# Optimization experiments

Hardware: AMD Instinct MI355X
Metric: run time of the kernel (lower is better)

Reference implementation:

```python
import jax, jax.numpy as jnp
import numpy as np

B, T, M, P = 512, 128, 512, 512


def setup_inputs() -> dict:
    key = jax.random.key(0)
    ks = jax.random.split(key, 20)
    g = lambda k, shape: (jax.random.normal(k, shape, dtype=jnp.float32) * 0.02)
    return {
        "encoded_inputs": jax.random.normal(ks[0], (B, T, M), dtype=jnp.float32),
        "y": jax.random.normal(ks[1], (B, T, 1), dtype=jnp.float32),
        # W_d: Linear(2P, M)
        "W_d_w": g(ks[2], (M, 2 * P)), "W_d_b": g(ks[3], (M,)),
        # U_d: Linear(M, M, bias=False)
        "U_d_w": g(ks[4], (M, M)),
        # v_d: Linear(M, 1, bias=False)
        "v_d_w": g(ks[5], (1, M)),
        # w_tilda: Linear(M+1, 1)
        "w_tilda_w": g(ks[6], (1, M + 1)), "w_tilda_b": g(ks[7], (1,)),
        # W_y: Linear(P+M, P)
        "W_y_w": g(ks[8], (P, P + M)), "W_y_b": g(ks[9], (P,)),
        # v_y: Linear(P, 1)
        "v_y_w": g(ks[10], (1, P)), "v_y_b": g(ks[11], (1,)),
        # LSTMCell(input_size=1, hidden_size=P); gate order i, f, g, o
        "W_ih": g(ks[12], (4 * P, 1)), "W_hh": g(ks[13], (4 * P, P)),
        "b_ih": g(ks[14], (4 * P,)), "b_hh": g(ks[15], (4 * P,)),
    }


def _forward(encoded_inputs, y, W_d_w, W_d_b, U_d_w, v_d_w, w_tilda_w, w_tilda_b,
             W_y_w, W_y_b, v_y_w, v_y_b, W_ih, W_hh, b_ih, b_hh):
    Bn = encoded_inputs.shape[0]
    # U_d(encoded_inputs) is identical at every timestep in the original loop; hoist it.
    Uy = jnp.einsum('btm,nm->btn', encoded_inputs, U_d_w)  # [B,T,M]

    def step(carry, y_t):
        d, s, _ = carry  # d: hidden [B,P], s: cell [B,P]
        x1 = jnp.concatenate([d, s], axis=1) @ W_d_w.T + W_d_b       # [B,M]
        z1 = jnp.tanh(x1[:, None, :] + Uy)                           # [B,T,M]
        l = jnp.einsum('btm,m->bt', z1, v_d_w[0])                    # [B,T]
        beta = jax.nn.softmax(l, axis=1)
        c_t = jnp.einsum('bt,btm->bm', beta, encoded_inputs)          # [B,M]
        y_tilda = jnp.concatenate([c_t, y_t], axis=1) @ w_tilda_w.T + w_tilda_b  # [B,1]
        gates = y_tilda @ W_ih.T + b_ih + d @ W_hh.T + b_hh          # [B,4P]
        i_g, f_g, g_g, o_g = jnp.split(gates, 4, axis=1)
        i_g = jax.nn.sigmoid(i_g); f_g = jax.nn.sigmoid(f_g)
        g_g = jnp.tanh(g_g); o_g = jax.nn.sigmoid(o_g)
        s_new = f_g * s + i_g * g_g
        d_new = o_g * jnp.tanh(s_new)
        return (d_new, s_new, c_t), None

    init = (jnp.zeros((Bn, P), encoded_inputs.dtype),
            jnp.zeros((Bn, P), encoded_inputs.dtype),
            jnp.zeros((Bn, M), encoded_inputs.dtype))
    (d_T, s_T, c_T), _ = jax.lax.scan(step, init, jnp.swapaxes(y, 0, 1))  # scan over T
    h = jnp.concatenate([d_T, c_T], axis=1) @ W_y_w.T + W_y_b            # [B,P]
    return h @ v_y_w.T + v_y_b                                           # [B,1]


def reference(encoded_inputs, y, W_d_w, W_d_b, U_d_w, v_d_w, w_tilda_w, w_tilda_b,
              W_y_w, W_y_b, v_y_w, v_y_b, W_ih, W_hh, b_ih, b_hh):
    return _forward(encoded_inputs, y, W_d_w, W_d_b, U_d_w, v_d_w, w_tilda_w,
                    w_tilda_b, W_y_w, W_y_b, v_y_w, v_y_b, W_ih, W_hh, b_ih, b_hh)
```

## Files before the change

kernel.cpp:

```cpp
#include <hip/hip_runtime.h>
#include <hip/hip_bf16.h>

#define Bsz 512
#define Tsz 128
#define Msz 512
#define Psz 512

typedef __attribute__((ext_vector_type(8))) unsigned short ushort8v;
typedef __attribute__((ext_vector_type(8))) short short8v;
typedef __attribute__((ext_vector_type(4))) float floatx4;

__device__ __forceinline__ float h2f(unsigned short u) {
    union { unsigned short u; _Float16 h; } c; c.u = u; return (float)c.h;
}
__device__ __forceinline__ unsigned short f2h(float f) {
    union { unsigned short u; _Float16 h; } c; c.h = (_Float16)f; return c.u;
}
__device__ __forceinline__ unsigned short f2bf(float f) {
    union { float f; unsigned int i; } c; c.f = f;
    unsigned int u = c.i;
    unsigned int r = u + 0x7fffu + ((u >> 16) & 1u);
    return (unsigned short)(r >> 16);
}
__device__ __forceinline__ float fast_tanh(float x) {
    x = fminf(fmaxf(x, -15.f), 15.f);
    float e = __expf(2.f * x);
    return 1.f - 2.f / (e + 1.f);
}
__device__ __forceinline__ float fast_sig(float x) {
    x = fminf(fmaxf(x, -30.f), 30.f);
    return 1.f / (1.f + __expf(-x));
}

__global__ __launch_bounds__(256) void k_uy(const float* __restrict__ A,
                                            const float* __restrict__ U,
                                            unsigned short* __restrict__ C) {
    __shared__ float As[32][68];
    __shared__ float Us[32][68];
    const int tid = threadIdx.x;
    const int tx = tid & 15, ty = tid >> 4;
    const size_t r0 = (size_t)blockIdx.y * 64;
    const int n0 = blockIdx.x * 64;
    float acc[4][4] = {};
    for (int k0 = 0; k0 < 512; k0 += 32) {
#pragma unroll
        for (int i = 0; i < 2; ++i) {
            int f = tid + i * 256;
            int r = f >> 3;
            int kc = (f & 7) * 4;
            float4 v = *reinterpret_cast<const float4*>(&A[(r0 + r) * 512 + k0 + kc]);
            As[kc + 0][r] = v.x; As[kc + 1][r] = v.y; As[kc + 2][r] = v.z; As[kc + 3][r] = v.w;
            float4 w = *reinterpret_cast<const float4*>(&U[(size_t)(n0 + r) * 512 + k0 + kc]);
            Us[kc + 0][r] = w.x; Us[kc + 1][r] = w.y; Us[kc + 2][r] = w.z; Us[kc + 3][r] = w.w;
        }
        __syncthreads();
#pragma unroll
        for (int k = 0; k < 32; ++k) {
            float4 a = *reinterpret_cast<const float4*>(&As[k][ty * 4]);
            float4 b = *reinterpret_cast<const float4*>(&Us[k][tx * 4]);
            float av[4] = {a.x, a.y, a.z, a.w};
            float bv[4] = {b.x, b.y, b.z, b.w};
#pragma unroll
            for (int i = 0; i < 4; ++i)
#pragma unroll
                for (int j = 0; j < 4; ++j)
                    acc[i][j] = fmaf(av[i], bv[j], acc[i][j]);
        }
        __syncthreads();
    }
#pragma unroll
    for (int i = 0; i < 4; ++i) {
        size_t row = r0 + ty * 4 + i;
        ushort4 o;
        o.x = f2h(acc[i][0]); o.y = f2h(acc[i][1]);
        o.z = f2h(acc[i][2]); o.w = f2h(acc[i][3]);
        *reinterpret_cast<ushort4*>(&C[row * 512 + n0 + tx * 4]) = o;
    }
}

__global__ __launch_bounds__(256) void k_e2h(const float* __restrict__ e,
                                             unsigned short* __restrict__ o) {
    size_t i = ((size_t)blockIdx.x * 256 + threadIdx.x) * 8;
    float4 a = *reinterpret_cast<const float4*>(e + i);
    float4 b = *reinterpret_cast<const float4*>(e + i + 4);
    ushort8v r;
    r[0] = f2h(a.x); r[1] = f2h(a.y); r[2] = f2h(a.z); r[3] = f2h(a.w);
    r[4] = f2h(b.x); r[5] = f2h(b.y); r[6] = f2h(b.z); r[7] = f2h(b.w);
    *reinterpret_cast<ushort8v*>(o + i) = r;
}

__global__ __launch_bounds__(256) void k_w2b(const float* __restrict__ Whh,
                                             const float* __restrict__ Wdw,
                                             unsigned short* __restrict__ W16) {
    size_t o = ((size_t)blockIdx.x * 256 + threadIdx.x) * 8;
    int row = (int)(o >> 9), k = (int)(o & 511);
    const float* src;
    if (row < 2048)      src = &Whh[(size_t)row * 512 + k];
    else if (row < 2560) src = &Wdw[(size_t)(row - 2048) * 1024 + k];
    else                 src = &Wdw[(size_t)(row - 2560) * 1024 + 512 + k];
    float4 a = *reinterpret_cast<const float4*>(src);
    float4 b = *reinterpret_cast<const float4*>(src + 4);
    ushort8v r;
    r[0] = f2bf(a.x); r[1] = f2bf(a.y); r[2] = f2bf(a.z); r[3] = f2bf(a.w);
    r[4] = f2bf(b.x); r[5] = f2bf(b.y); r[6] = f2bf(b.z); r[7] = f2bf(b.w);
    *reinterpret_cast<ushort8v*>(W16 + o) = r;
}

__global__ void k_zero(float* a, float* b, unsigned short* ah, unsigned short* bh, int n) {
    int i = blockIdx.x * blockDim.x + threadIdx.x;
    if (i < n) { a[i] = 0.f; b[i] = 0.f; ah[i] = 0; bh[i] = 0; }
}

__global__ __launch_bounds__(256) void k_mm(const unsigned short* __restrict__ dbh,
                                            const unsigned short* __restrict__ sbh,
                                            const unsigned short* __restrict__ W16,
                                            const float* __restrict__ Wdb,
                                            float* __restrict__ gacc,
                                            float* __restrict__ x1g) {
    __shared__ unsigned short As[64][48];
    __shared__ unsigned short Ws[64][48];
    const int tid = threadIdx.x;
    const int lane = tid & 63, w = tid >> 6;
    const int rbw = (w >> 1) * 32, cbw = (w & 1) * 32;
    const int b0 = blockIdx.y * 64;
    const int n0 = blockIdx.x * 64;
    const bool isx1 = (n0 >= 2048);
    const int l15 = lane & 15, kq = (lane >> 4) * 8;
    floatx4 acc00 = {}, acc01 = {}, acc10 = {}, acc11 = {};

    const int npass = isx1 ? 2 : 1;
    for (int pass = 0; pass < npass; ++pass) {
        const unsigned short* Ab = (pass == 0) ? dbh : sbh;
        const unsigned short* Wb = W16 + (size_t)(pass == 0 ? n0 : n0 + 512) * 512;
        for (int k0 = 0; k0 < 512; k0 += 32) {
            {
                const int r = tid >> 2, kc = (tid & 3) * 8;
                *reinterpret_cast<ushort8v*>(&As[r][kc]) =
                    *reinterpret_cast<const ushort8v*>(&Ab[(size_t)(b0 + r) * 512 + k0 + kc]);
                *reinterpret_cast<ushort8v*>(&Ws[r][kc]) =
                    *reinterpret_cast<const ushort8v*>(&Wb[(size_t)r * 512 + k0 + kc]);
            }
            __syncthreads();
            short8v a0 = *reinterpret_cast<const short8v*>(&As[rbw + l15][kq]);
            short8v a1 = *reinterpret_cast<const short8v*>(&As[rbw + 16 + l15][kq]);
            short8v q0 = *reinterpret_cast<const short8v*>(&Ws[cbw + l15][kq]);
            short8v q1 = *reinterpret_cast<const short8v*>(&Ws[cbw + 16 + l15][kq]);
            acc00 = __builtin_amdgcn_mfma_f32_16x16x32_bf16(a0, q0, acc00, 0, 0, 0);
            acc01 = __builtin_amdgcn_mfma_f32_16x16x32_bf16(a0, q1, acc01, 0, 0, 0);
            acc10 = __builtin_amdgcn_mfma_f32_16x16x32_bf16(a1, q0, acc10, 0, 0, 0);
            acc11 = __builtin_amdgcn_mfma_f32_16x16x32_bf16(a1, q1, acc11, 0, 0, 0);
            __syncthreads();
        }
    }
    const int rB = rbw + (lane >> 4) * 4;
#pragma unroll
    for (int fr = 0; fr < 2; ++fr)
#pragma unroll
        for (int fc = 0; fc < 2; ++fc) {
            const floatx4 av = fr ? (fc ? acc11 : acc10) : (fc ? acc01 : acc00);
            const int col = cbw + fc * 16 + l15;
#pragma unroll
            for (int i = 0; i < 4; ++i) {
                const int row = b0 + rB + fr * 16 + i;
                if (!isx1) {
                    gacc[(size_t)row * 2048 + n0 + col] = av[i];
                } else {
                    const int m = (n0 - 2048) + col;
                    x1g[(size_t)row * 512 + m] = av[i] + Wdb[m];
                }
            }
        }
}

__global__ __launch_bounds__(512) void k_attn2(const unsigned short* __restrict__ Uyh,
                                               const unsigned short* __restrict__ ench,
                                               const float* __restrict__ encf,
                                               const float* __restrict__ x1g,
                                               const float* __restrict__ vd,
                                               const float* __restrict__ wt,
                                               const float* __restrict__ wtb,
                                               const float* __restrict__ yin,
                                               const float* __restrict__ gacc,
                                               const float* __restrict__ Wih,
                                               const float* __restrict__ bih,
                                               const float* __restrict__ bhh,
                                               const float* __restrict__ scur,
                                               float* __restrict__ snxt,
                                               float* __restrict__ dnxt,
                                               unsigned short* __restrict__ snh,
                                               unsigned short* __restrict__ dnh,
                                               float* __restrict__ cout,
                                               int tstep, int useh) {
    __shared__ float x1_s[512];
    __shared__ float l_s[128];
    __shared__ float pacc[8][512];
    __shared__ float sred[8];
    __shared__ float y_bc;
    const int tid = threadIdx.x, b = blockIdx.x;
    const int w = tid >> 6, lane = tid & 63;
    x1_s[tid] = x1g[(size_t)b * 512 + tid];
    __syncthreads();
    {
        const int mb = lane * 8;
        float4 xa = *reinterpret_cast<const float4*>(&x1_s[mb]);
        float4 xb = *reinterpret_cast<const float4*>(&x1_s[mb + 4]);
        float4 va = *reinterpret_cast<const float4*>(&vd[mb]);
        float4 vb = *reinterpret_cast<const float4*>(&vd[mb + 4]);
        const unsigned short* ubase = Uyh + (size_t)b * 128 * 512 + mb;
#pragma unroll 2
        for (int tt = 0; tt < 16; ++tt) {
            const int t = w * 16 + tt;
            ushort8v u = *reinterpret_cast<const ushort8v*>(ubase + (size_t)t * 512);
            float s;
            s  = fast_tanh(h2f(u[0]) + xa.x) * va.x;
            s += fast_tanh(h2f(u[1]) + xa.y) * va.y;
            s += fast_tanh(h2f(u[2]) + xa.z) * va.z;
            s += fast_tanh(h2f(u[3]) + xa.w) * va.w;
            s += fast_tanh(h2f(u[4]) + xb.x) * vb.x;
            s += fast_tanh(h2f(u[5]) + xb.y) * vb.y;
            s += fast_tanh(h2f(u[6]) + xb.z) * vb.z;
            s += fast_tanh(h2f(u[7]) + xb.w) * vb.w;
#pragma unroll
            for (int off = 32; off; off >>= 1) s += __shfl_xor(s, off);
            if (lane == 0) l_s[t] = s;
        }
    }
    __syncthreads();
    if (tid < 64) {
        float v0 = l_s[tid], v1 = l_s[tid + 64];
        float mx = fmaxf(v0, v1);
#pragma unroll
        for (int off = 32; off; off >>= 1) mx = fmaxf(mx, __shfl_xor(mx, off));
        float e0 = __expf(v0 - mx), e1 = __expf(v1 - mx);
        float sm = e0 + e1;
#pragma unroll
        for (int off = 32; off; off >>= 1) sm += __shfl_xor(sm, off);
        float inv = 1.f / sm;
        l_s[tid] = e0 * inv; l_s[tid + 64] = e1 * inv;
    }
    __syncthreads();
    float a0 = 0.f, a1 = 0.f, a2 = 0.f, a3 = 0.f, a4 = 0.f, a5 = 0.f, a6 = 0.f, a7 = 0.f;
    if (useh) {
        const unsigned short* eb = ench + (size_t)b * (Tsz * Msz) + lane * 8;
#pragma unroll
        for (int tt = 0; tt < 16; ++tt) {
            const int t = tt * 8 + w;
            ushort8v uu = *reinterpret_cast<const ushort8v*>(eb + (size_t)t * 512);
            const float bt = l_s[t];
            a0 = fmaf(bt, h2f(uu[0]), a0); a1 = fmaf(bt, h2f(uu[1]), a1);
            a2 = fmaf(bt, h2f(uu[2]), a2); a3 = fmaf(bt, h2f(uu[3]), a3);
            a4 = fmaf(bt, h2f(uu[4]), a4); a5 = fmaf(bt, h2f(uu[5]), a5);
            a6 = fmaf(bt, h2f(uu[6]), a6); a7 = fmaf(bt, h2f(uu[7]), a7);
        }
    } else {
        const float* eb = encf + (size_t)b * (Tsz * Msz) + lane * 8;
#pragma unroll
        for (int tt = 0; tt < 16; ++tt) {
            const int t = tt * 8 + w;
            float4 e0 = *reinterpret_cast<const float4*>(eb + (size_t)t * 512);
            float4 e1 = *reinterpret_cast<const float4*>(eb + (size_t)t * 512 + 4);
            const float bt = l_s[t];
            a0 = fmaf(bt, e0.x, a0); a1 = fmaf(bt, e0.y, a1);
            a2 = fmaf(bt, e0.z, a2); a3 = fmaf(bt, e0.w, a3);
            a4 = fmaf(bt, e1.x, a4); a5 = fmaf(bt, e1.y, a5);
            a6 = fmaf(bt, e1.z, a6); a7 = fmaf(bt, e1.w, a7);
        }
    }
    float* pr = &pacc[w][lane * 8];
    *reinterpret_cast<float4*>(pr)     = make_float4(a0, a1, a2, a3);
    *reinterpret_cast<float4*>(pr + 4) = make_float4(a4, a5, a6, a7);
    __syncthreads();
    float c = pacc[0][tid];
#pragma unroll
    for (int ww = 1; ww < 8; ++ww) c += pacc[ww][tid];
    cout[(size_t)b * 512 + tid] = c;
    float part = c * wt[tid];
#pragma unroll
    for (int off = 32; off; off >>= 1) part += __shfl_xor(part, off);
    if (lane == 0) sred[w] = part;
    __syncthreads();
    if (tid == 0) {
        float tot = sred[0] + sred[1] + sred[2] + sred[3] +
                    sred[4] + sred[5] + sred[6] + sred[7];
        y_bc = tot + yin[(size_t)b * 128 + tstep] * wt[512] + wtb[0];
    }
    __syncthreads();
    {
        const float yt = y_bc;
        const int p = tid;
        const int e = b * 512 + p;
        const float* ga = gacc + (size_t)b * 2048;
        float gi = ga[p]        + yt * Wih[p]        + bih[p]        + bhh[p];
        float gf = ga[512 + p]  + yt * Wih[512 + p]  + bih[512 + p]  + bhh[512 + p];
        float gg = ga[1024 + p] + yt * Wih[1024 + p] + bih[1024 + p] + bhh[1024 + p];
        float go = ga[1536 + p] + yt * Wih[1536 + p] + bih[1536 + p] + bhh[1536 + p];
        float sv = fast_sig(gf) * scur[e] + fast_sig(gi) * fast_tanh(gg);
        float dv = fast_sig(go) * fast_tanh(sv);
        snxt[e] = sv; dnxt[e] = dv;
        snh[e] = f2bf(sv); dnh[e] = f2bf(dv);
    }
}

__global__ __launch_bounds__(256) void k_final(const float* __restrict__ dfin,
                                               const float* __restrict__ cfin,
                                               const float* __restrict__ Wy,
                                               const float* __restrict__ Wyb,
                                               const float* __restrict__ vy,
                                               const float* __restrict__ vyb,
                                               float* __restrict__ out) {
    __shared__ float hc[1024];
    __shared__ float sred[8];
    const int tid = threadIdx.x, b = blockIdx.x;
    hc[tid] = dfin[(size_t)b * 512 + tid];
    hc[256 + tid] = dfin[(size_t)b * 512 + 256 + tid];
    hc[512 + tid] = cfin[(size_t)b * 512 + tid];
    hc[768 + tid] = cfin[(size_t)b * 512 + 256 + tid];
    __syncthreads();
    float part = 0.f;
#pragma unroll
    for (int pi = 0; pi < 2; ++pi) {
        int p = tid + pi * 256;
        float acc = Wyb[p];
        const float* wr = Wy + (size_t)p * 1024;
#pragma unroll 4
        for (int k = 0; k < 1024; k += 4) {
            float4 w = *reinterpret_cast<const float4*>(&wr[k]);
            acc = fmaf(hc[k], w.x, acc);
            acc = fmaf(hc[k + 1], w.y, acc);
            acc = fmaf(hc[k + 2], w.z, acc);
            acc = fmaf(hc[k + 3], w.w, acc);
        }
        part += acc * vy[p];
    }
#pragma unroll
    for (int off = 32; off; off >>= 1) part += __shfl_xor(part, off);
    const int lane = tid & 63, wid = tid >> 6;
    if (lane == 0) sred[wid] = part;
    __syncthreads();
    if (tid == 0) out[b] = sred[0] + sred[1] + sred[2] + sred[3] + vyb[0];
}

extern "C" void kernel_launch(void* const* d_in, const int* in_sizes, int n_in,
                              void* d_out, int out_size, void* d_ws, size_t ws_size,
                              hipStream_t stream) {
    const float* enc = (const float*)d_in[0];
    const float* yin = (const float*)d_in[1];
    const float* Wdw = (const float*)d_in[2];
    const float* Wdb = (const float*)d_in[3];
    const float* Udw = (const float*)d_in[4];
    const float* vdw = (const float*)d_in[5];
    const float* wtw = (const float*)d_in[6];
    const float* wtb = (const float*)d_in[7];
    const float* Wyw = (const float*)d_in[8];
    const float* Wyb = (const float*)d_in[9];
    const float* vyw = (const float*)d_in[10];
    const float* vyb = (const float*)d_in[11];
    const float* Wih = (const float*)d_in[12];
    const float* Whh = (const float*)d_in[13];
    const float* bih = (const float*)d_in[14];
    const float* bhh = (const float*)d_in[15];
    float* out = (float*)d_out;
    const int N = Bsz * Psz;

    char* p = (char*)d_ws;
    unsigned short* Uyh = (unsigned short*)p;  p += (size_t)Bsz * Tsz * Msz * 2;
    unsigned short* W16 = (unsigned short*)p;  p += (size_t)3072 * 512 * 2;
    unsigned short* dbh = (unsigned short*)p;  p += (size_t)2 * N * 2;
    unsigned short* sbh = (unsigned short*)p;  p += (size_t)2 * N * 2;
    float* dbuf = (float*)p;  p += (size_t)2 * N * 4;
    float* sbuf = (float*)p;  p += (size_t)2 * N * 4;
    float* x1g  = (float*)p;  p += (size_t)N * 4;
    float* cb   = (float*)p;  p += (size_t)N * 4;
    float* gacc = (float*)p;  p += (size_t)Bsz * 2048 * 4;
    unsigned short* ench = (unsigned short*)p;
    const size_t need = (size_t)((char*)(ench + (size_t)Bsz * Tsz * Msz) - (char*)d_ws);
    const int useh = (ws_size >= need) ? 1 : 0;

    k_uy<<<dim3(Msz / 64, (Bsz * Tsz) / 64), 256, 0, stream>>>(enc, Udw, Uyh);
    if (useh)
        k_e2h<<<(Bsz * Tsz * Msz) / (256 * 8), 256, 0, stream>>>(enc, ench);
    k_w2b<<<(3072 * 512) / (256 * 8), 256, 0, stream>>>(Whh, Wdw, W16);
    k_zero<<<(N + 255) / 256, 256, 0, stream>>>(dbuf, sbuf, dbh, sbh, N);

    for (int t = 0; t < Tsz; ++t) {
        const int c = t & 1, n = c ^ 1;
        k_mm<<<dim3(40, 8), 256, 0, stream>>>(dbh + (size_t)c * N, sbh + (size_t)c * N,
                                              W16, Wdb, gacc, x1g);
        k_attn2<<<Bsz, 512, 0, stream>>>(Uyh, ench, enc, x1g, vdw, wtw, wtb, yin,
                                         gacc, Wih, bih, bhh,
                                         sbuf + (size_t)c * N,
                                         sbuf + (size_t)n * N, dbuf + (size_t)n * N,
                                         sbh + (size_t)n * N, dbh + (size_t)n * N,
                                         cb, t, useh);
    }
    k_final<<<Bsz, 256, 0, stream>>>(dbuf, cb, Wyw, Wyb, vyw, vyb, out);
}
```

Baseline: 7.292 ms.

## Precompute encoder·w_tilda projection and only build context vector at last step

Since y_tilda = beta·(enc·w_tilda[:M]) + ..., the per-step context vector reduction over the full [T,M] encoder tile is replaced by a dot product of beta with a precomputed [B,T] projection computed once in a new kernel. The full weighted sum over encoder states is now only performed at the final timestep, where c_T is needed for the output head. This removes reading the fp16 encoder copy every step, drops the fp16 conversion kernel, and changes the summation order of y_tilda slightly.

```diff
diff --git a/kernel.cpp b/kernel.cpp
--- a/kernel.cpp
+++ b/kernel.cpp
@@ -78,15 +78,22 @@
     }
 }
 
-__global__ __launch_bounds__(256) void k_e2h(const float* __restrict__ e,
-                                             unsigned short* __restrict__ o) {
-    size_t i = ((size_t)blockIdx.x * 256 + threadIdx.x) * 8;
-    float4 a = *reinterpret_cast<const float4*>(e + i);
-    float4 b = *reinterpret_cast<const float4*>(e + i + 4);
-    ushort8v r;
-    r[0] = f2h(a.x); r[1] = f2h(a.y); r[2] = f2h(a.z); r[3] = f2h(a.w);
-    r[4] = f2h(b.x); r[5] = f2h(b.y); r[6] = f2h(b.z); r[7] = f2h(b.w);
-    *reinterpret_cast<ushort8v*>(o + i) = r;
+__global__ __launch_bounds__(256) void k_ewt(const float* __restrict__ enc,
+                                             const float* __restrict__ wt,
+                                             float* __restrict__ ewt) {
+    const int lane = threadIdx.x & 63;
+    const int pair = blockIdx.x * 4 + (threadIdx.x >> 6);
+    const float* e = enc + (size_t)pair * 512 + lane * 8;
+    float4 a = *reinterpret_cast<const float4*>(e);
+    float4 b = *reinterpret_cast<const float4*>(e + 4);
+    const float* wp = wt + lane * 8;
+    float4 w0 = *reinterpret_cast<const float4*>(wp);
+    float4 w1 = *reinterpret_cast<const float4*>(wp + 4);
+    float s = a.x * w0.x + a.y * w0.y + a.z * w0.z + a.w * w0.w +
+              b.x * w1.x + b.y * w1.y + b.z * w1.z + b.w * w1.w;
+#pragma unroll
+    for (int off = 32; off; off >>= 1) s += __shfl_xor(s, off);
+    if (lane == 0) ewt[pair] = s;
 }
 
 __global__ __launch_bounds__(256) void k_w2b(const float* __restrict__ Whh,
@@ -172,9 +179,9 @@
         }
 }
 
-__global__ __launch_bounds__(512) void k_attn2(const unsigned short* __restrict__ Uyh,
-                                               const unsigned short* __restrict__ ench,
+__global__ __launch_bounds__(512) void k_attn3(const unsigned short* __restrict__ Uyh,
                                                const float* __restrict__ encf,
+                                               const float* __restrict__ ewt,
                                                const float* __restrict__ x1g,
                                                const float* __restrict__ vd,
                                                const float* __restrict__ wt,
@@ -190,11 +197,10 @@
                                                unsigned short* __restrict__ snh,
                                                unsigned short* __restrict__ dnh,
                                                float* __restrict__ cout,
-                                               int tstep, int useh) {
+                                               int tstep) {
     __shared__ float x1_s[512];
     __shared__ float l_s[128];
     __shared__ float pacc[8][512];
-    __shared__ float sred[8];
     __shared__ float y_bc;
     const int tid = threadIdx.x, b = blockIdx.x;
     const int w = tid >> 6, lane = tid & 63;
@@ -239,21 +245,17 @@
         l_s[tid] = e0 * inv; l_s[tid + 64] = e1 * inv;
     }
     __syncthreads();
-    float a0 = 0.f, a1 = 0.f, a2 = 0.f, a3 = 0.f, a4 = 0.f, a5 = 0.f, a6 = 0.f, a7 = 0.f;
-    if (useh) {
-        const unsigned short* eb = ench + (size_t)b * (Tsz * Msz) + lane * 8;
-#pragma unroll
-        for (int tt = 0; tt < 16; ++tt) {
-            const int t = tt * 8 + w;
-            ushort8v uu = *reinterpret_cast<const ushort8v*>(eb + (size_t)t * 512);
-            const float bt = l_s[t];
-            a0 = fmaf(bt, h2f(uu[0]), a0); a1 = fmaf(bt, h2f(uu[1]), a1);
-            a2 = fmaf(bt, h2f(uu[2]), a2); a3 = fmaf(bt, h2f(uu[3]), a3);
-            a4 = fmaf(bt, h2f(uu[4]), a4); a5 = fmaf(bt, h2f(uu[5]), a5);
-            a6 = fmaf(bt, h2f(uu[6]), a6); a7 = fmaf(bt, h2f(uu[7]), a7);
-        }
-    } else {
+    if (w == 0) {
+        const float* er = ewt + b * 128;
+        float pp = l_s[lane] * er[lane] + l_s[lane + 64] * er[lane + 64];
+#pragma unroll
+        for (int off = 32; off; off >>= 1) pp += __shfl_xor(pp, off);
+        if (lane == 0)
+            y_bc = pp + yin[(size_t)b * 128 + tstep] * wt[512] + wtb[0];
+    }
+    if (tstep == Tsz - 1) {
         const float* eb = encf + (size_t)b * (Tsz * Msz) + lane * 8;
+        float a0 = 0.f, a1 = 0.f, a2 = 0.f, a3 = 0.f, a4 = 0.f, a5 = 0.f, a6 = 0.f, a7 = 0.f;
 #pragma unroll
         for (int tt = 0; tt < 16; ++tt) {
             const int t = tt * 8 + w;
@@ -265,26 +267,17 @@
             a4 = fmaf(bt, e1.x, a4); a5 = fmaf(bt, e1.y, a5);
             a6 = fmaf(bt, e1.z, a6); a7 = fmaf(bt, e1.w, a7);
         }
-    }
-    float* pr = &pacc[w][lane * 8];
-    *reinterpret_cast<float4*>(pr)     = make_float4(a0, a1, a2, a3);
-    *reinterpret_cast<float4*>(pr + 4) = make_float4(a4, a5, a6, a7);
-    __syncthreads();
-    float c = pacc[0][tid];
-#pragma unroll
-    for (int ww = 1; ww < 8; ++ww) c += pacc[ww][tid];
-    cout[(size_t)b * 512 + tid] = c;
-    float part = c * wt[tid];
-#pragma unroll
-    for (int off = 32; off; off >>= 1) part += __shfl_xor(part, off);
-    if (lane == 0) sred[w] = part;
-    __syncthreads();
-    if (tid == 0) {
-        float tot = sred[0] + sred[1] + sred[2] + sred[3] +
-                    sred[4] + sred[5] + sred[6] + sred[7];
-        y_bc = tot + yin[(size_t)b * 128 + tstep] * wt[512] + wtb[0];
-    }
-    __syncthreads();
+        float* pr = &pacc[w][lane * 8];
+        *reinterpret_cast<float4*>(pr)     = make_float4(a0, a1, a2, a3);
+        *reinterpret_cast<float4*>(pr + 4) = make_float4(a4, a5, a6, a7);
+    }
+    __syncthreads();
+    if (tstep == Tsz - 1) {
+        float c = pacc[0][tid];
+#pragma unroll
+        for (int ww = 1; ww < 8; ++ww) c += pacc[ww][tid];
+        cout[(size_t)b * 512 + tid] = c;
+    }
     {
         const float yt = y_bc;
         const int p = tid;
@@ -372,13 +365,10 @@
     float* x1g  = (float*)p;  p += (size_t)N * 4;
     float* cb   = (float*)p;  p += (size_t)N * 4;
     float* gacc = (float*)p;  p += (size_t)Bsz * 2048 * 4;
-    unsigned short* ench = (unsigned short*)p;
-    const size_t need = (size_t)((char*)(ench + (size_t)Bsz * Tsz * Msz) - (char*)d_ws);
-    const int useh = (ws_size >= need) ? 1 : 0;
+    float* ewt  = (float*)p;  p += (size_t)Bsz * Tsz * 4;
 
     k_uy<<<dim3(Msz / 64, (Bsz * Tsz) / 64), 256, 0, stream>>>(enc, Udw, Uyh);
-    if (useh)
-        k_e2h<<<(Bsz * Tsz * Msz) / (256 * 8), 256, 0, stream>>>(enc, ench);
+    k_ewt<<<(Bsz * Tsz) / 4, 256, 0, stream>>>(enc, wtw, ewt);
     k_w2b<<<(3072 * 512) / (256 * 8), 256, 0, stream>>>(Whh, Wdw, W16);
     k_zero<<<(N + 255) / 256, 256, 0, stream>>>(dbuf, sbuf, dbh, sbh, N);
 
@@ -386,12 +376,12 @@
         const int c = t & 1, n = c ^ 1;
         k_mm<<<dim3(40, 8), 256, 0, stream>>>(dbh + (size_t)c * N, sbh + (size_t)c * N,
                                               W16, Wdb, gacc, x1g);
-        k_attn2<<<Bsz, 512, 0, stream>>>(Uyh, ench, enc, x1g, vdw, wtw, wtb, yin,
+        k_attn3<<<Bsz, 512, 0, stream>>>(Uyh, enc, ewt, x1g, vdw, wtw, wtb, yin,
                                          gacc, Wih, bih, bhh,
                                          sbuf + (size_t)c * N,
                                          sbuf + (size_t)n * N, dbuf + (size_t)n * N,
                                          sbh + (size_t)n * N, dbh + (size_t)n * N,
-                                         cb, t, useh);
+                                         cb, t);
     }
     k_final<<<Bsz, 256, 0, stream>>>(dbuf, cb, Wyw, Wyb, vyw, vyb, out);
 }
```

After: 6.441 ms. 11.7% less time.
